# Performance work log

Hardware: AMD Instinct MI355X
Metric: run time of the kernel (lower is better)

## Reference

```python
import jax, jax.numpy as jnp
import numpy as np

B, E, D = 4096, 64, 1024

def setup_inputs() -> dict:
    key = jax.random.key(0)
    k1, k2 = jax.random.split(key)
    z = jax.random.normal(k1, (B, D), dtype=jnp.float32)
    expert_keys = jax.random.normal(k2, (E, D), dtype=jnp.float32)
    log_sigma = jnp.zeros((D,), dtype=jnp.float32)
    return {"z": z, "expert_keys": expert_keys, "log_sigma": log_sigma}

def reference(z, expert_keys, log_sigma):
    # diag(sigma_inv) @ diff followed by (. * diff).sum(-1) is exactly an
    # elementwise-scaled squared distance: sum_d exp(-log_sigma_d) * diff_d^2
    sigma_inv = jnp.exp(-log_sigma)                              # [D]
    diff = z[:, None, :] - expert_keys[None, :, :]               # [B, E, D]
    mahalanobis_dist = jnp.einsum('bed,d,bed->be', diff, sigma_inv, diff)  # [B, E]
    similarity = 1.0 / (1.0 + mahalanobis_dist)                  # [B, E]
    weights = jax.nn.softmax(similarity, axis=-1)                # [B, E]
    weighted_expert = weights @ expert_keys                      # [B, D]
    return (similarity, weighted_expert)
```

## Files before the change

### kernel.cpp

```cpp
#include <hip/hip_runtime.h>
#include <hip/hip_bf16.h>

#define B_N 4096
#define E_N 64
#define D_N 1024
#define ROWS 16

typedef __bf16 bf16x8 __attribute__((ext_vector_type(8)));
typedef __bf16 bf16x4 __attribute__((ext_vector_type(4)));
typedef float f32x4 __attribute__((ext_vector_type(4)));


__global__ __launch_bounds__(256) void prep_kernel(
    const float* __restrict__ keys, const float* __restrict__ lsig,
    float* __restrict__ sinv, float* __restrict__ ak,
    __bf16* __restrict__ sk, __bf16* __restrict__ kT)
{
  __shared__ float red[4];
  __shared__ __bf16 tl[64][72];
  const int bid = blockIdx.x;
  const int t = threadIdx.x;

  if (bid < 64) {
    const int e = bid;
    const float4 k4 = *(const float4*)(keys + e * D_N + 4 * t);
    const float4 l4 = *(const float4*)(lsig + 4 * t);
    float4 s4;
    s4.x = expf(-l4.x); s4.y = expf(-l4.y); s4.z = expf(-l4.z); s4.w = expf(-l4.w);
    if (e == 0) *(float4*)(sinv + 4 * t) = s4;
    const float4 sk4 = make_float4(s4.x * k4.x, s4.y * k4.y, s4.z * k4.z, s4.w * k4.w);
    bf16x4 skb;
    skb[0] = (__bf16)sk4.x; skb[1] = (__bf16)sk4.y; skb[2] = (__bf16)sk4.z; skb[3] = (__bf16)sk4.w;
    *(bf16x4*)(sk + e * D_N + 4 * t) = skb;
    float p = sk4.x * k4.x + sk4.y * k4.y + sk4.z * k4.z + sk4.w * k4.w;
    #pragma unroll
    for (int off = 32; off > 0; off >>= 1) p += __shfl_down(p, off);
    if ((t & 63) == 0) red[t >> 6] = p;
    __syncthreads();
    if (t == 0) ak[e] = red[0] + red[1] + red[2] + red[3];
  } else {
    const int d0 = (bid - 64) * 64;
    #pragma unroll
    for (int p = 0; p < 4; ++p) {
      const int e  = p * 16 + (t >> 4);
      const int dd = (t & 15) * 4;
      const float4 k4 = *(const float4*)(keys + (size_t)e * D_N + d0 + dd);
      tl[dd + 0][e] = (__bf16)k4.x; tl[dd + 1][e] = (__bf16)k4.y;
      tl[dd + 2][e] = (__bf16)k4.z; tl[dd + 3][e] = (__bf16)k4.w;
    }
    __syncthreads();
    #pragma unroll
    for (int p = 0; p < 2; ++p) {
      const int dd = p * 32 + (t >> 3);
      const int l8 = t & 7;
      const bf16x8 v = *(const bf16x8*)&tl[dd][l8 * 8];
      *(bf16x8*)(kT + (size_t)(d0 + dd) * E_N + l8 * 8) = v;
    }
  }
}

__global__ __launch_bounds__(1024) void main_kernel(
    const float* __restrict__ z, const float* __restrict__ sinv,
    const float* __restrict__ ak, const __bf16* __restrict__ sk,
    const __bf16* __restrict__ kT,
    float* __restrict__ out_sim, float* __restrict__ out_we)
{
  constexpr int ZS = D_N + 8;
  __shared__ __bf16 zlds[ROWS * ZS];
  __shared__ float azs[ROWS];
  __shared__ float pacc[4][4][16][20];
  __shared__ __bf16 wlds[ROWS][72];

  const int t  = threadIdx.x;
  const int b0 = blockIdx.x * ROWS;

  const int wave = t >> 6;
  const int lane = t & 63;
  const int ln = lane & 15;
  const int q  = lane >> 4;
  const int et = wave & 3;
  const int kq = wave >> 2;

  f32x4 ak4 = {0.f, 0.f, 0.f, 0.f};
  if (t < 256) ak4 = *(const f32x4*)(ak + (t & 15) * 4);

  const int sr = wave;
  const int sc = lane;
  const float* zrow = z + (size_t)(b0 + sr) * D_N;
  float az = 0.f;
  #pragma unroll
  for (int l = 0; l < 4; ++l) {
    const int c = sc * 4 + l * 256;
    const float4 z4 = *(const float4*)(zrow + c);
    const float4 s4 = *(const float4*)(sinv + c);
    az += s4.x * z4.x * z4.x + s4.y * z4.y * z4.y + s4.z * z4.z * z4.z + s4.w * z4.w * z4.w;
    bf16x4 zb;
    zb[0] = (__bf16)z4.x; zb[1] = (__bf16)z4.y; zb[2] = (__bf16)z4.z; zb[3] = (__bf16)z4.w;
    *(bf16x4*)(&zlds[sr * ZS + c]) = zb;
  }
  az += __shfl_xor(az, 1);  az += __shfl_xor(az, 2);
  az += __shfl_xor(az, 4);  az += __shfl_xor(az, 8);
  az += __shfl_xor(az, 16); az += __shfl_xor(az, 32);
  if (sc == 0) azs[sr] = az;

  __syncthreads();

  const __bf16* bp = sk + (size_t)(et * 16 + ln) * D_N + kq * 256 + q * 8;
  const __bf16* ap = &zlds[ln * ZS + kq * 256 + q * 8];
  f32x4 acc = {0.f, 0.f, 0.f, 0.f};
  #pragma unroll
  for (int ks = 0; ks < 8; ++ks) {
    const bf16x8 bfr = *(const bf16x8*)(bp + ks * 32);
    const bf16x8 afr = *(const bf16x8*)(ap + ks * 32);
    acc = __builtin_amdgcn_mfma_f32_16x16x32_bf16(afr, bfr, acc, 0, 0, 0);
  }
  #pragma unroll
  for (int i = 0; i < 4; ++i) pacc[kq][et][q * 4 + i][ln] = acc[i];

  __syncthreads();

  if (t < 256) {
    const int row = t >> 4, seg = t & 15;
    const int pe = seg >> 2, pc = (seg & 3) * 4;
    f32x4 p = *(const f32x4*)&pacc[0][pe][row][pc];
    #pragma unroll
    for (int k = 1; k < 4; ++k) {
      const f32x4 pk = *(const f32x4*)&pacc[k][pe][row][pc];
      p[0] += pk[0]; p[1] += pk[1]; p[2] += pk[2]; p[3] += pk[3];
    }
    const float azr = azs[row];
    f32x4 s;
    #pragma unroll
    for (int j = 0; j < 4; ++j) {
      const float dist = azr + ak4[j] - 2.0f * p[j];
      s[j] = 1.0f / (1.0f + dist);
    }
    *(f32x4*)(out_sim + (size_t)(b0 + row) * E_N + seg * 4) = s;
    float mx = fmaxf(fmaxf(s[0], s[1]), fmaxf(s[2], s[3]));
    mx = fmaxf(mx, __shfl_xor(mx, 1));
    mx = fmaxf(mx, __shfl_xor(mx, 2));
    mx = fmaxf(mx, __shfl_xor(mx, 4));
    mx = fmaxf(mx, __shfl_xor(mx, 8));
    float v[4];
    float sum = 0.f;
    #pragma unroll
    for (int j = 0; j < 4; ++j) { v[j] = __expf(s[j] - mx); sum += v[j]; }
    sum += __shfl_xor(sum, 1);
    sum += __shfl_xor(sum, 2);
    sum += __shfl_xor(sum, 4);
    sum += __shfl_xor(sum, 8);
    const float inv = 1.0f / sum;
    bf16x4 wq;
    #pragma unroll
    for (int j = 0; j < 4; ++j) wq[j] = (__bf16)(v[j] * inv);
    *(bf16x4*)&wlds[row][seg * 4] = wq;
  }
  __syncthreads();

  const bf16x8 a0 = *(const bf16x8*)&wlds[ln][q * 8];
  const bf16x8 a1 = *(const bf16x8*)&wlds[ln][32 + q * 8];
  #pragma unroll
  for (int i = 0; i < 4; ++i) {
    const int dt = wave + 16 * i;
    const int d0 = dt * 16;
    const __bf16* kp = kT + (size_t)(d0 + ln) * E_N + q * 8;
    const bf16x8 b0f = *(const bf16x8*)(kp);
    const bf16x8 b1f = *(const bf16x8*)(kp + 32);
    f32x4 o = {0.f, 0.f, 0.f, 0.f};
    o = __builtin_amdgcn_mfma_f32_16x16x32_bf16(a0, b0f, o, 0, 0, 0);
    o = __builtin_amdgcn_mfma_f32_16x16x32_bf16(a1, b1f, o, 0, 0, 0);
    #pragma unroll
    for (int j = 0; j < 4; ++j)
      out_we[(size_t)(b0 + q * 4 + j) * D_N + d0 + ln] = o[j];
  }
}

extern "C" void kernel_launch(void* const* d_in, const int* in_sizes, int n_in,
                              void* d_out, int out_size, void* d_ws, size_t ws_size,
                              hipStream_t stream)
{
  const float* z    = (const float*)d_in[0];
  const float* keys = (const float*)d_in[1];
  const float* ls   = (const float*)d_in[2];
  float* out_sim = (float*)d_out;
  float* out_we  = out_sim + (size_t)B_N * E_N;
  char* ws = (char*)d_ws;
  float*  sinv = (float*)(ws);
  float*  ak   = (float*)(ws + 4096);
  __bf16* sk   = (__bf16*)(ws + 4352);
  __bf16* kT   = (__bf16*)(ws + 135424);
  prep_kernel<<<80, 256, 0, stream>>>(keys, ls, sinv, ak, sk, kT);
  main_kernel<<<B_N / ROWS, 1024, 0, stream>>>(z, sinv, ak, sk, kT, out_sim, out_we);
}
```

Baseline: 81.55 us.

## Fuse prep and main kernels into one cooperative launch with grid sync

Merges the key-preprocessing kernel into the main kernel. The first 80 blocks compute the scaled bf16 keys, the key norms and the transposed keys, every block computes sigma_inv into LDS, and a cooperative grid-wide sync separates preprocessing from the MFMA stages. The aim is to remove the second kernel launch and the serialization between the two kernels, and to overlap loading z with the prep work. In exchange it needs a cooperative launch, where all 256 blocks of 1024 threads must be co-resident, and it pays for a grid barrier.

```diff
diff --git a/kernel.cpp b/kernel.cpp
--- a/kernel.cpp
+++ b/kernel.cpp
@@ -1,5 +1,8 @@
 #include <hip/hip_runtime.h>
 #include <hip/hip_bf16.h>
+#include <hip/hip_cooperative_groups.h>
+
+namespace cg = cooperative_groups;
 
 #define B_N 4096
 #define E_N 64
@@ -11,68 +14,24 @@
 typedef float f32x4 __attribute__((ext_vector_type(4)));
 
 
-__global__ __launch_bounds__(256) void prep_kernel(
-    const float* __restrict__ keys, const float* __restrict__ lsig,
-    float* __restrict__ sinv, float* __restrict__ ak,
-    __bf16* __restrict__ sk, __bf16* __restrict__ kT)
-{
-  __shared__ float red[4];
-  __shared__ __bf16 tl[64][72];
-  const int bid = blockIdx.x;
-  const int t = threadIdx.x;
-
-  if (bid < 64) {
-    const int e = bid;
-    const float4 k4 = *(const float4*)(keys + e * D_N + 4 * t);
-    const float4 l4 = *(const float4*)(lsig + 4 * t);
-    float4 s4;
-    s4.x = expf(-l4.x); s4.y = expf(-l4.y); s4.z = expf(-l4.z); s4.w = expf(-l4.w);
-    if (e == 0) *(float4*)(sinv + 4 * t) = s4;
-    const float4 sk4 = make_float4(s4.x * k4.x, s4.y * k4.y, s4.z * k4.z, s4.w * k4.w);
-    bf16x4 skb;
-    skb[0] = (__bf16)sk4.x; skb[1] = (__bf16)sk4.y; skb[2] = (__bf16)sk4.z; skb[3] = (__bf16)sk4.w;
-    *(bf16x4*)(sk + e * D_N + 4 * t) = skb;
-    float p = sk4.x * k4.x + sk4.y * k4.y + sk4.z * k4.z + sk4.w * k4.w;
-    #pragma unroll
-    for (int off = 32; off > 0; off >>= 1) p += __shfl_down(p, off);
-    if ((t & 63) == 0) red[t >> 6] = p;
-    __syncthreads();
-    if (t == 0) ak[e] = red[0] + red[1] + red[2] + red[3];
-  } else {
-    const int d0 = (bid - 64) * 64;
-    #pragma unroll
-    for (int p = 0; p < 4; ++p) {
-      const int e  = p * 16 + (t >> 4);
-      const int dd = (t & 15) * 4;
-      const float4 k4 = *(const float4*)(keys + (size_t)e * D_N + d0 + dd);
-      tl[dd + 0][e] = (__bf16)k4.x; tl[dd + 1][e] = (__bf16)k4.y;
-      tl[dd + 2][e] = (__bf16)k4.z; tl[dd + 3][e] = (__bf16)k4.w;
-    }
-    __syncthreads();
-    #pragma unroll
-    for (int p = 0; p < 2; ++p) {
-      const int dd = p * 32 + (t >> 3);
-      const int l8 = t & 7;
-      const bf16x8 v = *(const bf16x8*)&tl[dd][l8 * 8];
-      *(bf16x8*)(kT + (size_t)(d0 + dd) * E_N + l8 * 8) = v;
-    }
-  }
-}
-
-__global__ __launch_bounds__(1024) void main_kernel(
-    const float* __restrict__ z, const float* __restrict__ sinv,
-    const float* __restrict__ ak, const __bf16* __restrict__ sk,
-    const __bf16* __restrict__ kT,
+__global__ __launch_bounds__(1024) void fused_kernel(
+    const float* __restrict__ z, const float* __restrict__ keys,
+    const float* __restrict__ lsig,
+    float* __restrict__ ak, __bf16* __restrict__ sk, __bf16* __restrict__ kT,
     float* __restrict__ out_sim, float* __restrict__ out_we)
 {
   constexpr int ZS = D_N + 8;
+  __shared__ float sinv_lds[D_N];
+  __shared__ float red[16];
+  __shared__ __bf16 tl[64][72];
   __shared__ __bf16 zlds[ROWS * ZS];
   __shared__ float azs[ROWS];
   __shared__ float pacc[4][4][16][20];
   __shared__ __bf16 wlds[ROWS][72];
 
-  const int t  = threadIdx.x;
-  const int b0 = blockIdx.x * ROWS;
+  const int t   = threadIdx.x;
+  const int bid = blockIdx.x;
+  const int b0  = bid * ROWS;
 
   const int wave = t >> 6;
   const int lane = t & 63;
@@ -81,8 +40,40 @@
   const int et = wave & 3;
   const int kq = wave >> 2;
 
-  f32x4 ak4 = {0.f, 0.f, 0.f, 0.f};
-  if (t < 256) ak4 = *(const f32x4*)(ak + (t & 15) * 4);
+  sinv_lds[t] = __expf(-lsig[t]);
+  __syncthreads();
+
+  if (bid < 64) {
+    const int e = bid;
+    const float k = keys[(size_t)e * D_N + t];
+    const float s = sinv_lds[t];
+    sk[(size_t)e * D_N + t] = (__bf16)(s * k);
+    float p = s * k * k;
+    #pragma unroll
+    for (int off = 32; off > 0; off >>= 1) p += __shfl_down(p, off);
+    if (lane == 0) red[wave] = p;
+    __syncthreads();
+    if (t == 0) {
+      float a = 0.f;
+      #pragma unroll
+      for (int i = 0; i < 16; ++i) a += red[i];
+      ak[e] = a;
+    }
+  } else if (bid < 80) {
+    const int d0 = (bid - 64) * 64;
+    const int e  = t >> 4;
+    const int dd = (t & 15) * 4;
+    const float4 k4 = *(const float4*)(keys + (size_t)e * D_N + d0 + dd);
+    tl[dd + 0][e] = (__bf16)k4.x; tl[dd + 1][e] = (__bf16)k4.y;
+    tl[dd + 2][e] = (__bf16)k4.z; tl[dd + 3][e] = (__bf16)k4.w;
+    __syncthreads();
+    if (t < 512) {
+      const int d8 = t >> 3;
+      const int l8 = t & 7;
+      const bf16x8 v = *(const bf16x8*)&tl[d8][l8 * 8];
+      *(bf16x8*)(kT + (size_t)(d0 + d8) * E_N + l8 * 8) = v;
+    }
+  }
 
   const int sr = wave;
   const int sc = lane;
@@ -92,8 +83,8 @@
   for (int l = 0; l < 4; ++l) {
     const int c = sc * 4 + l * 256;
     const float4 z4 = *(const float4*)(zrow + c);
-    const float4 s4 = *(const float4*)(sinv + c);
-    az += s4.x * z4.x * z4.x + s4.y * z4.y * z4.y + s4.z * z4.z * z4.z + s4.w * z4.w * z4.w;
+    const f32x4 s4 = *(const f32x4*)(&sinv_lds[c]);
+    az += s4[0] * z4.x * z4.x + s4[1] * z4.y * z4.y + s4[2] * z4.z * z4.z + s4[3] * z4.w * z4.w;
     bf16x4 zb;
     zb[0] = (__bf16)z4.x; zb[1] = (__bf16)z4.y; zb[2] = (__bf16)z4.z; zb[3] = (__bf16)z4.w;
     *(bf16x4*)(&zlds[sr * ZS + c]) = zb;
@@ -103,7 +94,10 @@
   az += __shfl_xor(az, 16); az += __shfl_xor(az, 32);
   if (sc == 0) azs[sr] = az;
 
-  __syncthreads();
+  cg::this_grid().sync();
+
+  f32x4 ak4 = {0.f, 0.f, 0.f, 0.f};
+  if (t < 256) ak4 = *(const f32x4*)(ak + (t & 15) * 4);
 
   const __bf16* bp = sk + (size_t)(et * 16 + ln) * D_N + kq * 256 + q * 8;
   const __bf16* ap = &zlds[ln * ZS + kq * 256 + q * 8];
@@ -185,10 +179,14 @@
   float* out_sim = (float*)d_out;
   float* out_we  = out_sim + (size_t)B_N * E_N;
   char* ws = (char*)d_ws;
-  float*  sinv = (float*)(ws);
-  float*  ak   = (float*)(ws + 4096);
-  __bf16* sk   = (__bf16*)(ws + 4352);
-  __bf16* kT   = (__bf16*)(ws + 135424);
-  prep_kernel<<<80, 256, 0, stream>>>(keys, ls, sinv, ak, sk, kT);
-  main_kernel<<<B_N / ROWS, 1024, 0, stream>>>(z, sinv, ak, sk, kT, out_sim, out_we);
+  float*  ak   = (float*)(ws);
+  __bf16* sk   = (__bf16*)(ws + 256);
+  __bf16* kT   = (__bf16*)(ws + 131328);
+
+  void* args[] = { (void*)&z, (void*)&keys, (void*)&ls,
+                   (void*)&ak, (void*)&sk, (void*)&kT,
+                   (void*)&out_sim, (void*)&out_we };
+  hipLaunchCooperativeKernel((void*)fused_kernel,
+                             dim3(B_N / ROWS), dim3(1024),
+                             args, 0, stream);
 }
```

New measurement: 126.1 us. 54.6% more time.
